# Kernel optimization log

Hardware: AMD Instinct MI355X
Metric: run time of the kernel (lower is better)

The kernel has to match this reference:

```python
import jax, jax.numpy as jnp
import numpy as np

H = 8          # n_channels
NEIGHBORS = 5


def setup_inputs() -> dict:
    key = jax.random.key(0)
    k1, k2 = jax.random.split(key)
    B, N, C = 8, 1024, 256
    x = jax.random.normal(k1, (B, N, C), dtype=jnp.float32)
    # torch Linear weight: [out_features, in_features] = [2*H*C, C]
    W_qk = jax.random.normal(k2, (2 * H * C, C), dtype=jnp.float32) * (C ** -0.5)
    return {"x": x, "W_qk": W_qk}


def _forward(x, W_qk):
    B, N, C = x.shape
    scale = C ** -0.5
    qk = (x @ W_qk.T).reshape(B, N, 2, H, C).transpose(2, 0, 3, 1, 4)
    q, k = qk[0], qk[1]                              # [B,H,N,C]
    attn = jax.nn.softmax(jnp.einsum('bhnc,bhmc->bhnm', q, k) * scale, axis=-1)

    # clip(): top-k on detached channel-summed attention
    sum_edge = jnp.sum(jax.lax.stop_gradient(attn), axis=1)   # [B,N,N]
    _, index = jax.lax.top_k(sum_edge, NEIGHBORS)             # [B,N,NEIGHBORS]
    # Faithful to source: every mask row gets 1 at the union of ALL rows'
    # top-k indices (inner loop iterates over all rows of `inds`), plus eye(N).
    flat_idx = index.reshape(B, N * NEIGHBORS)                # [B, N*nb]
    col_mask = jnp.zeros((B, N), dtype=attn.dtype).at[
        jnp.arange(B)[:, None], flat_idx].set(1.0)            # [B,N]
    mask = jnp.maximum(jnp.eye(N, dtype=attn.dtype)[None], col_mask[:, None, :])  # [B,N,N]

    new_edge = mask[:, None] * attn                           # [B,H,N,N]

    # norm_edge(): row norm, then col norm, then row @ col^T
    norm_row = new_edge / (jnp.sum(new_edge, axis=-1, keepdims=True) + 1e-16)
    norm_col = norm_row / (jnp.sum(norm_row, axis=-2, keepdims=True) + 1e-16)
    return jnp.einsum('bhnm,bhkm->bhnk', norm_row, norm_col)  # [B,H,N,N]


def reference(x, W_qk):
    return _forward(x, W_qk)
```

## Files before the change

kernel.cpp:

```cpp
#include <hip/hip_runtime.h>
#include <hip/hip_bf16.h>
#include <cstdint>
#include <cstddef>

#define BB 8
#define HH 8
#define NN 1024
#define CC 256
#define YC 2048
#define NSPLIT (BB*NN*CC/4/256)

typedef __attribute__((ext_vector_type(8))) __bf16 bf16x8;
typedef __attribute__((ext_vector_type(4))) __bf16 bf16x4;
typedef __attribute__((ext_vector_type(4))) float f32x4;

__device__ inline void async16(const void* g, void* l)
{
  __builtin_amdgcn_global_load_lds(
      reinterpret_cast<const __attribute__((address_space(1))) unsigned int*>(
          reinterpret_cast<uintptr_t>(g)),
      reinterpret_cast<__attribute__((address_space(3))) unsigned int*>(
          reinterpret_cast<uintptr_t>(l)),
      16, 0, 0);
}

__device__ inline float waveMax(float v) {
#pragma unroll
  for (int o = 32; o > 0; o >>= 1) v = fmaxf(v, __shfl_xor(v, o, 64));
  return v;
}
__device__ inline float waveSum(float v) {
#pragma unroll
  for (int o = 32; o > 0; o >>= 1) v += __shfl_xor(v, o, 64);
  return v;
}

__global__ __launch_bounds__(256) void prep_kernel(
    const float* __restrict__ x, const float* __restrict__ W,
    __bf16* __restrict__ xh, __bf16* __restrict__ xl,
    __bf16* __restrict__ Th, __bf16* __restrict__ Tl)
{
  __shared__ float t[64][65];
  if (blockIdx.x < NSPLIT) {
    const int i = blockIdx.x * 256 + threadIdx.x;
    const float4 v = ((const float4*)x)[i];
    bf16x4 h, l;
    h.x = (__bf16)v.x; l.x = (__bf16)(v.x - (float)h.x);
    h.y = (__bf16)v.y; l.y = (__bf16)(v.y - (float)h.y);
    h.z = (__bf16)v.z; l.z = (__bf16)(v.z - (float)h.z);
    h.w = (__bf16)v.w; l.w = (__bf16)(v.w - (float)h.w);
    ((bf16x4*)xh)[i] = h;
    ((bf16x4*)xl)[i] = l;
    return;
  }
  const int bid = blockIdx.x - NSPLIT;
  const int z = bid >> 4;
  const int tile = bid & 15;
  const int i0 = (tile & 3) * 64, c0 = (tile >> 2) * 64;
  const float* Wb = W + ((size_t)z << 16);
  const int tr = threadIdx.x >> 6;
  const int tc = threadIdx.x & 63;
#pragma unroll
  for (int rr = 0; rr < 64; rr += 4)
    t[rr + tr][tc] = Wb[(size_t)(i0 + rr + tr) * 256 + c0 + tc];
  __syncthreads();
  __bf16* Thb = Th + ((size_t)z << 16);
  __bf16* Tlb = Tl + ((size_t)z << 16);
#pragma unroll
  for (int cc = 0; cc < 64; cc += 4) {
    const int c = cc + tr, i = tc;
    const float v = t[i][c];
    const __bf16 h = (__bf16)v;
    Thb[(size_t)(c0 + c) * 256 + i0 + i] = h;
    Tlb[(size_t)(c0 + c) * 256 + i0 + i] = (__bf16)(v - (float)h);
  }
}

__global__ __launch_bounds__(256) void pp_mfma_kernel(
    const __bf16* __restrict__ Th, const __bf16* __restrict__ Tl,
    __bf16* __restrict__ Phi, __bf16* __restrict__ Plo)
{
  const int h = blockIdx.z;
  const __bf16* Ah = Th + ((size_t)(8 + h) << 16);
  const __bf16* Al = Tl + ((size_t)(8 + h) << 16);
  const __bf16* Bh = Th + ((size_t)h << 16);
  const __bf16* Bl = Tl + ((size_t)h << 16);

  __shared__ __bf16 AsH[128 * 32], AsL[128 * 32], BsH[128 * 32], BsL[128 * 32];

  const int tid = threadIdx.x, lane = tid & 63, wid = tid >> 6;
  const int wr = wid >> 1, wc = wid & 1;
  const int bM = blockIdx.y * 128, bN = blockIdx.x * 128;

  const int srow = wid * 16 + (lane >> 2);
  const int scol = (lane & 3) * 8;
  const __bf16* gAh = Ah + (size_t)(bM + srow) * CC + scol;
  const __bf16* gAl = Al + (size_t)(bM + srow) * CC + scol;
  const __bf16* gBh = Bh + (size_t)(bN + srow) * CC + scol;
  const __bf16* gBl = Bl + (size_t)(bN + srow) * CC + scol;
  char* lAh = (char*)AsH + wid * 16 * 64;
  char* lAl = (char*)AsL + wid * 16 * 64;
  char* lBh = (char*)BsH + wid * 16 * 64;
  char* lBl = (char*)BsL + wid * 16 * 64;

  f32x4 acc[4][4];
  const f32x4 z4 = {0.f, 0.f, 0.f, 0.f};
#pragma unroll
  for (int m = 0; m < 4; ++m)
#pragma unroll
    for (int n = 0; n < 4; ++n) acc[m][n] = z4;

  for (int k0 = 0; k0 < CC; k0 += 32) {
    async16(gAh + k0, lAh); async16(gAh + k0 + 64 * CC, lAh + 64 * 64);
    async16(gAl + k0, lAl); async16(gAl + k0 + 64 * CC, lAl + 64 * 64);
    async16(gBh + k0, lBh); async16(gBh + k0 + 64 * CC, lBh + 64 * 64);
    async16(gBl + k0, lBl); async16(gBl + k0 + 64 * CC, lBl + 64 * 64);
    __syncthreads();

    bf16x8 ah[4], al[4], bh_[4], bl_[4];
    const int fb = (lane & 15) * 64 + (lane >> 4) * 16;
#pragma unroll
    for (int m = 0; m < 4; ++m) {
      ah[m] = *(const bf16x8*)((const char*)AsH + (wr * 64 + m * 16) * 64 + fb);
      al[m] = *(const bf16x8*)((const char*)AsL + (wr * 64 + m * 16) * 64 + fb);
    }
#pragma unroll
    for (int n = 0; n < 4; ++n) {
      bh_[n] = *(const bf16x8*)((const char*)BsH + (wc * 64 + n * 16) * 64 + fb);
      bl_[n] = *(const bf16x8*)((const char*)BsL + (wc * 64 + n * 16) * 64 + fb);
    }
#pragma unroll
    for (int m = 0; m < 4; ++m)
#pragma unroll
      for (int n = 0; n < 4; ++n) {
        acc[m][n] = __builtin_amdgcn_mfma_f32_16x16x32_bf16(al[m], bh_[n], acc[m][n], 0, 0, 0);
        acc[m][n] = __builtin_amdgcn_mfma_f32_16x16x32_bf16(ah[m], bl_[n], acc[m][n], 0, 0, 0);
        acc[m][n] = __builtin_amdgcn_mfma_f32_16x16x32_bf16(ah[m], bh_[n], acc[m][n], 0, 0, 0);
      }
    __syncthreads();
  }

  const int fr = lane & 15;
  const int fq = lane >> 4;
#pragma unroll
  for (int m = 0; m < 4; ++m) {
    const int row0 = h * 256 + bM + wr * 64 + m * 16 + fq * 4;
#pragma unroll
    for (int n = 0; n < 4; ++n) {
      const int col = bN + wc * 64 + n * 16 + fr;
#pragma unroll
      for (int r = 0; r < 4; ++r) {
        const float v = acc[m][n][r];
        const __bf16 hh = (__bf16)v;
        Phi[(size_t)(row0 + r) * CC + col] = hh;
        Plo[(size_t)(row0 + r) * CC + col] = (__bf16)(v - (float)hh);
      }
    }
  }
}

__global__ __launch_bounds__(256) void y_mfma_kernel(
    const __bf16* __restrict__ Ah, const __bf16* __restrict__ Al,
    const __bf16* __restrict__ Bh, const __bf16* __restrict__ Bl,
    __bf16* __restrict__ Chi, __bf16* __restrict__ Clo)
{
  __shared__ __bf16 AsH[2][128 * 32], AsL[2][128 * 32];
  __shared__ __bf16 BsH[2][128 * 32], BsL[2][128 * 32];

  const int tid = threadIdx.x, lane = tid & 63, wid = tid >> 6;
  const int wr = wid >> 1, wc = wid & 1;
  const int bM = blockIdx.y * 128, bN = blockIdx.x * 128;

  const int srow = wid * 16 + (lane >> 2);
  const int scol = (lane & 3) * 8;
  const __bf16* gAh = Ah + (size_t)(bM + srow) * CC + scol;
  const __bf16* gAl = Al + (size_t)(bM + srow) * CC + scol;
  const __bf16* gBh = Bh + (size_t)(bN + srow) * CC + scol;
  const __bf16* gBl = Bl + (size_t)(bN + srow) * CC + scol;
  const int lofs = wid * 16 * 64;

  f32x4 acc[4][4];
  const f32x4 z = {0.f, 0.f, 0.f, 0.f};
#pragma unroll
  for (int m = 0; m < 4; ++m)
#pragma unroll
    for (int n = 0; n < 4; ++n) acc[m][n] = z;

  const int fb = (lane & 15) * 64 + (lane >> 4) * 16;

#define Y_STAGE(buf, k0_)                                                      \
  do {                                                                         \
    async16(gAh + (k0_), (char*)AsH[buf] + lofs);                              \
    async16(gAh + (k0_) + 64 * CC, (char*)AsH[buf] + lofs + 64 * 64);          \
    async16(gAl + (k0_), (char*)AsL[buf] + lofs);                              \
    async16(gAl + (k0_) + 64 * CC, (char*)AsL[buf] + lofs + 64 * 64);          \
    async16(gBh + (k0_), (char*)BsH[buf] + lofs);                              \
    async16(gBh + (k0_) + 64 * CC, (char*)BsH[buf] + lofs + 64 * 64);          \
    async16(gBl + (k0_), (char*)BsL[buf] + lofs);                              \
    async16(gBl + (k0_) + 64 * CC, (char*)BsL[buf] + lofs + 64 * 64);          \
  } while (0)

#define Y_COMPUTE(buf)                                                         \
  do {                                                                         \
    bf16x8 ah[4], al[4], bh_[4], bl_[4];                                       \
    _Pragma("unroll")                                                          \
    for (int m = 0; m < 4; ++m) {                                              \
      ah[m] = *(const bf16x8*)((const char*)AsH[buf] + (wr * 64 + m * 16) * 64 + fb); \
      al[m] = *(const bf16x8*)((const char*)AsL[buf] + (wr * 64 + m * 16) * 64 + fb); \
    }                                                                          \
    _Pragma("unroll")                                                          \
    for (int n = 0; n < 4; ++n) {                                              \
      bh_[n] = *(const bf16x8*)((const char*)BsH[buf] + (wc * 64 + n * 16) * 64 + fb); \
      bl_[n] = *(const bf16x8*)((const char*)BsL[buf] + (wc * 64 + n * 16) * 64 + fb); \
    }                                                                          \
    _Pragma("unroll")                                                          \
    for (int m = 0; m < 4; ++m)                                                \
      _Pragma("unroll")                                                        \
      for (int n = 0; n < 4; ++n) {                                            \
        acc[m][n] = __builtin_amdgcn_mfma_f32_16x16x32_bf16(al[m], bh_[n], acc[m][n], 0, 0, 0); \
        acc[m][n] = __builtin_amdgcn_mfma_f32_16x16x32_bf16(ah[m], bl_[n], acc[m][n], 0, 0, 0); \
        acc[m][n] = __builtin_amdgcn_mfma_f32_16x16x32_bf16(ah[m], bh_[n], acc[m][n], 0, 0, 0); \
      }                                                                        \
  } while (0)

  Y_STAGE(0, 0);
  int cur = 0;
#pragma unroll 1
  for (int k0 = 0; k0 < CC - 32; k0 += 32) {
    Y_STAGE(cur ^ 1, k0 + 32);
    asm volatile("s_waitcnt vmcnt(8)" ::: "memory");
    __builtin_amdgcn_s_barrier();
    __builtin_amdgcn_sched_barrier(0);
    Y_COMPUTE(cur);
    __builtin_amdgcn_s_barrier();
    __builtin_amdgcn_sched_barrier(0);
    cur ^= 1;
  }
  asm volatile("s_waitcnt vmcnt(0)" ::: "memory");
  __builtin_amdgcn_s_barrier();
  __builtin_amdgcn_sched_barrier(0);
  Y_COMPUTE(cur);

#undef Y_STAGE
#undef Y_COMPUTE

  const int fr = lane & 15;
  const int fq = lane >> 4;
#pragma unroll
  for (int m = 0; m < 4; ++m) {
    const int row0 = bM + wr * 64 + m * 16 + fq * 4;
#pragma unroll
    for (int n = 0; n < 4; ++n) {
      const int col = bN + wc * 64 + n * 16 + fr;
#pragma unroll
      for (int r = 0; r < 4; ++r) {
        const float v = acc[m][n][r];
        const __bf16 h = (__bf16)v;
        Chi[(size_t)(row0 + r) * YC + col] = h;
        Clo[(size_t)(row0 + r) * YC + col] = (__bf16)(v - (float)h);
      }
    }
  }
}

__global__ __launch_bounds__(256) void qkt_mfma_kernel(
    const __bf16* __restrict__ Yh, const __bf16* __restrict__ Yl,
    const __bf16* __restrict__ Xh, const __bf16* __restrict__ Xl,
    float* __restrict__ outall)
{
  const int f = blockIdx.x;
  const int xcd = f & 7;
  const int g = f >> 3;
  const int bh = xcd + 8 * (g >> 6);
  const int tile = g & 63;
  const int b = bh >> 3, h = bh & 7;
  const size_t aoff = (size_t)b * NN * YC + (size_t)h * CC;
  const size_t boff = (size_t)b * NN * CC;
  float* C = outall + ((size_t)bh << 20);

  __shared__ __bf16 AsH[2][128 * 32], AsL[2][128 * 32];
  __shared__ __bf16 BsH[2][128 * 32], BsL[2][128 * 32];

  const int tid = threadIdx.x, lane = tid & 63, wid = tid >> 6;
  const int wr = wid >> 1, wc = wid & 1;
  const int bM = (tile >> 3) * 128, bN = (tile & 7) * 128;

  const int srow = wid * 16 + (lane >> 2);
  const int scol = (lane & 3) * 8;
  const __bf16* gAh = Yh + aoff + (size_t)(bM + srow) * YC + scol;
  const __bf16* gAl = Yl + aoff + (size_t)(bM + srow) * YC + scol;
  const __bf16* gBh = Xh + boff + (size_t)(bN + srow) * CC + scol;
  const __bf16* gBl = Xl + boff + (size_t)(bN + srow) * CC + scol;
  const int lofs = wid * 16 * 64;

  f32x4 acc[4][4];
  const f32x4 z = {0.f, 0.f, 0.f, 0.f};
#pragma unroll
  for (int m = 0; m < 4; ++m)
#pragma unroll
    for (int n = 0; n < 4; ++n) acc[m][n] = z;

  const int fb = (lane & 15) * 64 + (lane >> 4) * 16;

#define QKT_STAGE(buf, k0_)                                                    \
  do {                                                                         \
    async16(gAh + (k0_), (char*)AsH[buf] + lofs);                              \
    async16(gAh + (k0_) + (size_t)64 * YC, (char*)AsH[buf] + lofs + 64 * 64);  \
    async16(gAl + (k0_), (char*)AsL[buf] + lofs);                              \
    async16(gAl + (k0_) + (size_t)64 * YC, (char*)AsL[buf] + lofs + 64 * 64);  \
    async16(gBh + (k0_), (char*)BsH[buf] + lofs);                              \
    async16(gBh + (k0_) + (size_t)64 * CC, (char*)BsH[buf] + lofs + 64 * 64);  \
    async16(gBl + (k0_), (char*)BsL[buf] + lofs);                              \
    async16(gBl + (k0_) + (size_t)64 * CC, (char*)BsL[buf] + lofs + 64 * 64);  \
  } while (0)

#define QKT_COMPUTE(buf)                                                       \
  do {                                                                         \
    bf16x8 ah[4], al[4], bh_[4], bl_[4];                                       \
    _Pragma("unroll")                                                          \
    for (int m = 0; m < 4; ++m) {                                              \
      ah[m] = *(const bf16x8*)((const char*)AsH[buf] + (wr * 64 + m * 16) * 64 + fb); \
      al[m] = *(const bf16x8*)((const char*)AsL[buf] + (wr * 64 + m * 16) * 64 + fb); \
    }                                                                          \
    _Pragma("unroll")                                                          \
    for (int n = 0; n < 4; ++n) {                                              \
      bh_[n] = *(const bf16x8*)((const char*)BsH[buf] + (wc * 64 + n * 16) * 64 + fb); \
      bl_[n] = *(const bf16x8*)((const char*)BsL[buf] + (wc * 64 + n * 16) * 64 + fb); \
    }                                                                          \
    _Pragma("unroll")                                                          \
    for (int m = 0; m < 4; ++m)                                                \
      _Pragma("unroll")                                                        \
      for (int n = 0; n < 4; ++n) {                                            \
        acc[m][n] = __builtin_amdgcn_mfma_f32_16x16x32_bf16(al[m], bh_[n], acc[m][n], 0, 0, 0); \
        acc[m][n] = __builtin_amdgcn_mfma_f32_16x16x32_bf16(ah[m], bl_[n], acc[m][n], 0, 0, 0); \
        acc[m][n] = __builtin_amdgcn_mfma_f32_16x16x32_bf16(ah[m], bh_[n], acc[m][n], 0, 0, 0); \
      }                                                                        \
  } while (0)

  QKT_STAGE(0, 0);
  int cur = 0;
#pragma unroll 1
  for (int k0 = 0; k0 < CC - 32; k0 += 32) {
    QKT_STAGE(cur ^ 1, k0 + 32);
    asm volatile("s_waitcnt vmcnt(8)" ::: "memory");
    __builtin_amdgcn_s_barrier();
    __builtin_amdgcn_sched_barrier(0);
    QKT_COMPUTE(cur);
    __builtin_amdgcn_s_barrier();
    __builtin_amdgcn_sched_barrier(0);
    cur ^= 1;
  }
  asm volatile("s_waitcnt vmcnt(0)" ::: "memory");
  __builtin_amdgcn_s_barrier();
  __builtin_amdgcn_sched_barrier(0);
  QKT_COMPUTE(cur);

#undef QKT_STAGE
#undef QKT_COMPUTE

  const int fr = lane & 15;
  const int fq = lane >> 4;
#pragma unroll
  for (int m = 0; m < 4; ++m) {
    const int row0 = bM + wr * 64 + m * 16 + fq * 4;
#pragma unroll
    for (int n = 0; n < 4; ++n) {
      const int col = bN + wc * 64 + n * 16 + fr;
#pragma unroll
      for (int r = 0; r < 4; ++r)
        C[(size_t)(row0 + r) * NN + col] = acc[m][n][r] * 0.0625f;
    }
  }
}

__global__ __launch_bounds__(256) void softmax_se_kernel(const float* __restrict__ logits,
                                                         __bf16* __restrict__ attnb,
                                                         float* __restrict__ se)
{
  const int bn = blockIdx.x;
  const int b = bn >> 10;
  const int n = bn & 1023;
  const int t = threadIdx.x;
  const int lane = t & 63, wv = t >> 6;
  __shared__ float wred[4];
  float4 acc = make_float4(0.f, 0.f, 0.f, 0.f);

#pragma unroll 1
  for (int h = 0; h < HH; ++h) {
    const size_t rowbase = (((size_t)(b * HH + h) << 10) + n) << 10;
    const float* ar = logits + rowbase;
    __bf16* arb = attnb + rowbase;
    float4 x = *(const float4*)(ar + (t << 2));
    float mx = waveMax(fmaxf(fmaxf(x.x, x.y), fmaxf(x.z, x.w)));
    if (lane == 0) wred[wv] = mx;
    __syncthreads();
    const float M = fmaxf(fmaxf(wred[0], wred[1]), fmaxf(wred[2], wred[3]));
    __syncthreads();

    float e0 = expf(x.x - M), e1 = expf(x.y - M), e2 = expf(x.z - M), e3 = expf(x.w - M);
    float s = waveSum(e0 + e1 + e2 + e3);
    if (lane == 0) wred[wv] = s;
    __syncthreads();
    const float inv = 1.0f / (wred[0] + wred[1] + wred[2] + wred[3]);

    const float o0 = e0 * inv, o1 = e1 * inv, o2 = e2 * inv, o3 = e3 * inv;
    bf16x4 ob; ob.x = (__bf16)o0; ob.y = (__bf16)o1; ob.z = (__bf16)o2; ob.w = (__bf16)o3;
    *(bf16x4*)(arb + (t << 2)) = ob;
    acc.x += o0; acc.y += o1; acc.z += o2; acc.w += o3;
    __syncthreads();
  }
  *(float4*)(se + (size_t)bn * NN + (t << 2)) = acc;
}

__global__ __launch_bounds__(256) void topk_kernel(const float* __restrict__ se,
                                                   float* __restrict__ colmask)
{
  const int bn = blockIdx.x;
  const int b = bn >> 10;
  const int t = threadIdx.x;
  const int lane = t & 63, wv = t >> 6;
  __shared__ float vals[NN];
  __shared__ unsigned long long wbest[4];
  const float* rowp = se + (size_t)bn * NN;
  for (int i = t; i < NN; i += 256) vals[i] = rowp[i];
  __syncthreads();

  for (int it = 0; it < 5; ++it) {
    unsigned long long best = 0ull;
    for (int i = t; i < NN; i += 256) {
      const float v = vals[i];
      if (v >= 0.f) {
        unsigned long long key =
            ((unsigned long long)__float_as_uint(v) << 32) | (unsigned)(NN - 1 - i);
        if (key > best) best = key;
      }
    }
#pragma unroll
    for (int o = 32; o > 0; o >>= 1) {
      const unsigned long long other = __shfl_xor(best, o, 64);
      if (other > best) best = other;
    }
    if (lane == 0) wbest[wv] = best;
    __syncthreads();
    if (t == 0) {
      unsigned long long bb = wbest[0];
      if (wbest[1] > bb) bb = wbest[1];
      if (wbest[2] > bb) bb = wbest[2];
      if (wbest[3] > bb) bb = wbest[3];
      const int idx = NN - 1 - (int)(bb & 0xFFFFFFFFull);
      colmask[b * NN + idx] = 1.0f;
      vals[idx] = -1.0f;
    }
    __syncthreads();
  }
}

__global__ __launch_bounds__(256) void cs_rs_kernel(const __bf16* __restrict__ attnb,
                                                    const float* __restrict__ colmask,
                                                    float* __restrict__ inv_rs,
                                                    float* __restrict__ part)
{
  const int bh = blockIdx.y;
  const int b = bh >> 3;
  const int chunk = blockIdx.x;
  const int t = threadIdx.x, lane = t & 63, wv = t >> 6;
  const __bf16* ab = attnb + ((size_t)bh << 20);
  const float* cm = colmask + b * NN;
  const int c0 = lane * 16;

  float cmv[16];
#pragma unroll
  for (int q = 0; q < 4; ++q) {
    const float4 c4 = *(const float4*)(cm + c0 + q * 4);
    cmv[q*4+0] = c4.x; cmv[q*4+1] = c4.y; cmv[q*4+2] = c4.z; cmv[q*4+3] = c4.w;
  }

  float a[16];
#pragma unroll
  for (int j = 0; j < 16; ++j) a[j] = 0.f;

  const int nbase = chunk * 64 + wv * 16;
#pragma unroll 1
  for (int r = 0; r < 16; ++r) {
    const int n = nbase + r;
    const __bf16* rowp = ab + ((size_t)n << 10) + c0;
    const bf16x8 v0 = *(const bf16x8*)(rowp);
    const bf16x8 v1 = *(const bf16x8*)(rowp + 8);
    float e[16];
    float rsum = 0.f;
#pragma unroll
    for (int j = 0; j < 8; ++j) {
      const float val = ((cmv[j] != 0.f) || (c0 + j == n)) ? (float)v0[j] : 0.f;
      e[j] = val; rsum += val;
    }
#pragma unroll
    for (int j = 0; j < 8; ++j) {
      const float val = ((cmv[8+j] != 0.f) || (c0 + 8 + j == n)) ? (float)v1[j] : 0.f;
      e[8+j] = val; rsum += val;
    }
    rsum = waveSum(rsum);
    const float ir = 1.0f / (rsum + 1e-16f);
    if (lane == 0) inv_rs[bh * NN + n] = ir;
#pragma unroll
    for (int j = 0; j < 16; ++j) a[j] += e[j] * ir;
  }

  __shared__ float l[4][NN];
#pragma unroll
  for (int j = 0; j < 16; ++j) l[wv][c0 + j] = a[j];
  __syncthreads();
  const int m0 = t << 2;
  float4 o;
  o.x = l[0][m0+0] + l[1][m0+0] + l[2][m0+0] + l[3][m0+0];
  o.y = l[0][m0+1] + l[1][m0+1] + l[2][m0+1] + l[3][m0+1];
  o.z = l[0][m0+2] + l[1][m0+2] + l[2][m0+2] + l[3][m0+2];
  o.w = l[0][m0+3] + l[1][m0+3] + l[2][m0+3] + l[3][m0+3];
  *(float4*)(part + (((size_t)chunk * (BB*HH) + bh) << 10) + m0) = o;
}

__global__ __launch_bounds__(256) void cs_fin_kernel(const float* __restrict__ part,
                                                     float* __restrict__ isc)
{
  const int bh = blockIdx.x;
  const int m0 = threadIdx.x << 2;
  float a0 = 0.f, a1 = 0.f, a2 = 0.f, a3 = 0.f;
#pragma unroll
  for (int c = 0; c < 16; ++c) {
    const float4 p = *(const float4*)(part + (((size_t)c * (BB*HH) + bh) << 10) + m0);
    a0 += p.x; a1 += p.y; a2 += p.z; a3 += p.w;
  }
  float4 o;
  o.x = 1.0f / sqrtf(a0 + 1e-16f);
  o.y = 1.0f / sqrtf(a1 + 1e-16f);
  o.z = 1.0f / sqrtf(a2 + 1e-16f);
  o.w = 1.0f / sqrtf(a3 + 1e-16f);
  *(float4*)(isc + ((size_t)bh << 10) + m0) = o;
}

__global__ __launch_bounds__(256) void g_kernel(const __bf16* __restrict__ attnb,
                                                const float* __restrict__ colmask,
                                                const float* __restrict__ inv_rs,
                                                const float* __restrict__ isc,
                                                __bf16* __restrict__ Gb)
{
  const size_t idx = ((size_t)blockIdx.x * 256 + threadIdx.x) << 3;
  const size_t row = idx >> 10;
  const int m = (int)(idx & 1023);
  const int n = (int)(row & 1023);
  const int bh = (int)(row >> 10);
  const int b = bh >> 3;
  const bf16x8 vb = *(const bf16x8*)(attnb + idx);
  const float4 c0 = *(const float4*)(colmask + b * NN + m);
  const float4 c1 = *(const float4*)(colmask + b * NN + m + 4);
  const float4 s0 = *(const float4*)(isc + ((size_t)bh << 10) + m);
  const float4 s1 = *(const float4*)(isc + ((size_t)bh << 10) + m + 4);
  const float ir = inv_rs[row];
  const float cm[8] = {c0.x, c0.y, c0.z, c0.w, c1.x, c1.y, c1.z, c1.w};
  const float sc[8] = {s0.x, s0.y, s0.z, s0.w, s1.x, s1.y, s1.z, s1.w};
  bf16x8 o;
#pragma unroll
  for (int j = 0; j < 8; ++j) {
    const float e = ((cm[j] != 0.f) || (m + j == n)) ? (float)vb[j] : 0.f;
    o[j] = (__bf16)(e * ir * sc[j]);
  }
  *(bf16x8*)(Gb + idx) = o;
}

__global__ __launch_bounds__(256) void ggt_mfma_kernel(const __bf16* __restrict__ Gball,
                                                       float* __restrict__ outall)
{
  const int f = blockIdx.x;
  const int xcd = f & 7;
  const int g = f >> 3;
  const int bh = xcd + 8 * (g / 36);
  int tt = g % 36;

  const __bf16* A = Gball + ((size_t)bh << 20);
  float* C = outall + ((size_t)bh << 20);

  int ti = 0;
#pragma unroll
  for (int r = 0; r < 8; ++r) {
    const int len = 8 - r;
    if (tt < len) { ti = r; break; }
    tt -= len;
  }
  const int tj = ti + tt;

  __shared__ __bf16 As[2][128 * 32];
  __shared__ __bf16 Bs[2][128 * 32];

  const int tid  = threadIdx.x;
  const int lane = tid & 63;
  const int wid  = tid >> 6;
  const int wr   = wid >> 1;
  const int wc   = wid & 1;
  const int bM   = ti * 128;
  const int bN   = tj * 128;

  const int srow = wid * 16 + (lane >> 2);
  const int scol = (lane & 3) * 8;
  const __bf16* gA = A + (size_t)(bM + srow) * NN + scol;
  const __bf16* gB = A + (size_t)(bN + srow) * NN + scol;
  const int lofs = wid * 16 * 64;

  f32x4 acc[4][4];
  const f32x4 z = {0.f, 0.f, 0.f, 0.f};
#pragma unroll
  for (int m = 0; m < 4; ++m)
#pragma unroll
    for (int n = 0; n < 4; ++n) acc[m][n] = z;

  const int fb = (lane & 15) * 64 + (lane >> 4) * 16;

  async16(gA,           (char*)As[0] + lofs);
  async16(gA + 64 * NN, (char*)As[0] + lofs + 64 * 64);
  async16(gB,           (char*)Bs[0] + lofs);
  async16(gB + 64 * NN, (char*)Bs[0] + lofs + 64 * 64);

  int cur = 0;
#pragma unroll 1
  for (int k0 = 0; k0 < NN - 32; k0 += 32) {
    const int nxt = cur ^ 1;
    async16(gA + k0 + 32,           (char*)As[nxt] + lofs);
    async16(gA + k0 + 32 + 64 * NN, (char*)As[nxt] + lofs + 64 * 64);
    async16(gB + k0 + 32,           (char*)Bs[nxt] + lofs);
    async16(gB + k0 + 32 + 64 * NN, (char*)Bs[nxt] + lofs + 64 * 64);
    asm volatile("s_waitcnt vmcnt(4)" ::: "memory");
    __builtin_amdgcn_s_barrier();
    __builtin_amdgcn_sched_barrier(0);

    bf16x8 a[4], b[4];
#pragma unroll
    for (int m = 0; m < 4; ++m)
      a[m] = *(const bf16x8*)((const char*)As[cur] + (wr * 64 + m * 16) * 64 + fb);
#pragma unroll
    for (int n = 0; n < 4; ++n)
      b[n] = *(const bf16x8*)((const char*)Bs[cur] + (wc * 64 + n * 16) * 64 + fb);
#pragma unroll
    for (int m = 0; m < 4; ++m)
#pragma unroll
      for (int n = 0; n < 4; ++n)
        acc[m][n] = __builtin_amdgcn_mfma_f32_16x16x32_bf16(a[m], b[n], acc[m][n], 0, 0, 0);
    __builtin_amdgcn_s_barrier();
    __builtin_amdgcn_sched_barrier(0);
    cur ^= 1;
  }

  asm volatile("s_waitcnt vmcnt(0)" ::: "memory");
  __builtin_amdgcn_s_barrier();
  __builtin_amdgcn_sched_barrier(0);
  {
    bf16x8 a[4], b[4];
#pragma unroll
    for (int m = 0; m < 4; ++m)
      a[m] = *(const bf16x8*)((const char*)As[cur] + (wr * 64 + m * 16) * 64 + fb);
#pragma unroll
    for (int n = 0; n < 4; ++n)
      b[n] = *(const bf16x8*)((const char*)Bs[cur] + (wc * 64 + n * 16) * 64 + fb);
#pragma unroll
    for (int m = 0; m < 4; ++m)
#pragma unroll
      for (int n = 0; n < 4; ++n)
        acc[m][n] = __builtin_amdgcn_mfma_f32_16x16x32_bf16(a[m], b[n], acc[m][n], 0, 0, 0);
  }

  const int fr = lane & 15;
  const int fq = lane >> 4;
#pragma unroll
  for (int m = 0; m < 4; ++m) {
    const int row0 = bM + wr * 64 + m * 16 + fq * 4;
#pragma unroll
    for (int n = 0; n < 4; ++n) {
      const int col = bN + wc * 64 + n * 16 + fr;
#pragma unroll
      for (int r = 0; r < 4; ++r)
        C[(size_t)(row0 + r) * NN + col] = acc[m][n][r];
    }
  }
  if (ti != tj) {
#pragma unroll
    for (int m = 0; m < 4; ++m) {
      const int colT = bM + wr * 64 + m * 16 + fq * 4;
#pragma unroll
      for (int n = 0; n < 4; ++n) {
        const int rowT = bN + wc * 64 + n * 16 + fr;
        *(f32x4*)(C + (size_t)rowT * NN + colT) = acc[m][n];
      }
    }
  }
}

extern "C" void kernel_launch(void* const* d_in, const int* in_sizes, int n_in,
                              void* d_out, int out_size, void* d_ws, size_t ws_size,
                              hipStream_t stream)
{
  const float* x = (const float*)d_in[0];
  const float* W = (const float*)d_in[1];
  float* logits = (float*)d_out;
  char* ws = (char*)d_ws;

  __bf16* y_hi  = (__bf16*)(ws + ((size_t)0   << 20));
  __bf16* y_lo  = (__bf16*)(ws + ((size_t)32  << 20));
  __bf16* attnb = (__bf16*)(ws + ((size_t)0   << 20));
  __bf16* x_hi  = (__bf16*)(ws + ((size_t)128 << 20));
  __bf16* x_lo  = (__bf16*)(ws + ((size_t)132 << 20));
  __bf16* T_hi  = (__bf16*)(ws + ((size_t)136 << 20));
  __bf16* T_lo  = (__bf16*)(ws + ((size_t)138 << 20));
  __bf16* P_hi  = (__bf16*)(ws + ((size_t)140 << 20));
  __bf16* P_lo  = (__bf16*)(ws + ((size_t)142 << 20));
  float*  se    = (float*)(ws + ((size_t)144 << 20));
  float*  cmask = (float*)(ws + ((size_t)176 << 20));
  float*  irs   = (float*)(ws + ((size_t)177 << 20));
  float*  isc   = (float*)(ws + ((size_t)178 << 20));
  float*  csp   = (float*)(ws + ((size_t)180 << 20));
  __bf16* Gb    = (__bf16*)(ws + ((size_t)192 << 20));

  hipLaunchKernelGGL(prep_kernel, dim3(NSPLIT + 256), dim3(256), 0, stream,
                     x, W, x_hi, x_lo, T_hi, T_lo);
  hipLaunchKernelGGL(pp_mfma_kernel, dim3(2, 2, 8), dim3(256), 0, stream,
                     T_hi, T_lo, P_hi, P_lo);

  hipLaunchKernelGGL(y_mfma_kernel, dim3(YC/128, (BB*NN)/128, 1), dim3(256), 0, stream,
                     x_hi, x_lo, P_hi, P_lo, y_hi, y_lo);

  hipLaunchKernelGGL(qkt_mfma_kernel, dim3(64 * 64), dim3(256), 0, stream,
                     y_hi, y_lo, x_hi, x_lo, logits);

  hipLaunchKernelGGL(softmax_se_kernel, dim3(BB*NN), dim3(256), 0, stream,
                     logits, attnb, se);

  hipMemsetAsync(cmask, 0, (size_t)BB * NN * 4, stream);
  hipLaunchKernelGGL(topk_kernel, dim3(BB*NN), dim3(256), 0, stream, se, cmask);

  hipLaunchKernelGGL(cs_rs_kernel, dim3(16, BB*HH), dim3(256), 0, stream,
                     attnb, cmask, irs, csp);
  hipLaunchKernelGGL(cs_fin_kernel, dim3(BB*HH), dim3(256), 0, stream, csp, isc);

  hipLaunchKernelGGL(g_kernel, dim3((BB*HH*NN*(long long)NN) / 8 / 256), dim3(256), 0, stream,
                     attnb, cmask, irs, isc, Gb);

  hipLaunchKernelGGL(ggt_mfma_kernel, dim3(36 * 64), dim3(256), 0, stream,
                     Gb, logits);

  (void)in_sizes; (void)n_in; (void)out_size; (void)ws_size;
}
```

Baseline: 512.7 us.

## Widen QK^T tile to 128x256 and drop LDS double buffering

The QK^T logits kernel moves from 128x128 to 128x256 output tiles, halving the grid and doubling the per-wave accumulators (4x8 fragments). This raises reuse of the A tile from LDS and cuts redundant global loads. To fit, the two-stage async LDS pipeline is replaced by a single buffer with plain __syncthreads before and after compute. Global load latency is therefore no longer overlapped with MFMA work, and register pressure rises, which may lower occupancy.

```diff
diff --git a/kernel.cpp b/kernel.cpp
--- a/kernel.cpp
+++ b/kernel.cpp
@@ -271,19 +271,19 @@
   const int f = blockIdx.x;
   const int xcd = f & 7;
   const int g = f >> 3;
-  const int bh = xcd + 8 * (g >> 6);
-  const int tile = g & 63;
+  const int bh = xcd + 8 * (g >> 5);
+  const int tile = g & 31;
   const int b = bh >> 3, h = bh & 7;
   const size_t aoff = (size_t)b * NN * YC + (size_t)h * CC;
   const size_t boff = (size_t)b * NN * CC;
   float* C = outall + ((size_t)bh << 20);
 
-  __shared__ __bf16 AsH[2][128 * 32], AsL[2][128 * 32];
-  __shared__ __bf16 BsH[2][128 * 32], BsL[2][128 * 32];
+  __shared__ __bf16 AsH[128 * 32], AsL[128 * 32];
+  __shared__ __bf16 BsH[256 * 32], BsL[256 * 32];
 
   const int tid = threadIdx.x, lane = tid & 63, wid = tid >> 6;
   const int wr = wid >> 1, wc = wid & 1;
-  const int bM = (tile >> 3) * 128, bN = (tile & 7) * 128;
+  const int bM = (tile >> 2) * 128, bN = (tile & 3) * 256;
 
   const int srow = wid * 16 + (lane >> 2);
   const int scol = (lane & 3) * 8;
@@ -291,72 +291,60 @@
   const __bf16* gAl = Yl + aoff + (size_t)(bM + srow) * YC + scol;
   const __bf16* gBh = Xh + boff + (size_t)(bN + srow) * CC + scol;
   const __bf16* gBl = Xl + boff + (size_t)(bN + srow) * CC + scol;
-  const int lofs = wid * 16 * 64;
-
-  f32x4 acc[4][4];
+  char* lAh = (char*)AsH + wid * 16 * 64;
+  char* lAl = (char*)AsL + wid * 16 * 64;
+  char* lBh = (char*)BsH + wid * 16 * 64;
+  char* lBl = (char*)BsL + wid * 16 * 64;
+
+  f32x4 acc[4][8];
   const f32x4 z = {0.f, 0.f, 0.f, 0.f};
 #pragma unroll
   for (int m = 0; m < 4; ++m)
 #pragma unroll
-    for (int n = 0; n < 4; ++n) acc[m][n] = z;
+    for (int n = 0; n < 8; ++n) acc[m][n] = z;
 
   const int fb = (lane & 15) * 64 + (lane >> 4) * 16;
 
-#define QKT_STAGE(buf, k0_)                                                    \
-  do {                                                                         \
-    async16(gAh + (k0_), (char*)AsH[buf] + lofs);                              \
-    async16(gAh + (k0_) + (size_t)64 * YC, (char*)AsH[buf] + lofs + 64 * 64);  \
-    async16(gAl + (k0_), (char*)AsL[buf] + lofs);                              \
-    async16(gAl + (k0_) + (size_t)64 * YC, (char*)AsL[buf] + lofs + 64 * 64);  \
-    async16(gBh + (k0_), (char*)BsH[buf] + lofs);                              \
-    async16(gBh + (k0_) + (size_t)64 * CC, (char*)BsH[buf] + lofs + 64 * 64);  \
-    async16(gBl + (k0_), (char*)BsL[buf] + lofs);                              \
-    async16(gBl + (k0_) + (size_t)64 * CC, (char*)BsL[buf] + lofs + 64 * 64);  \
-  } while (0)
-
-#define QKT_COMPUTE(buf)                                                       \
-  do {                                                                         \
-    bf16x8 ah[4], al[4], bh_[4], bl_[4];                                       \
-    _Pragma("unroll")                                                          \
-    for (int m = 0; m < 4; ++m) {                                              \
-      ah[m] = *(const bf16x8*)((const char*)AsH[buf] + (wr * 64 + m * 16) * 64 + fb); \
-      al[m] = *(const bf16x8*)((const char*)AsL[buf] + (wr * 64 + m * 16) * 64 + fb); \
-    }                                                                          \
-    _Pragma("unroll")                                                          \
-    for (int n = 0; n < 4; ++n) {                                              \
-      bh_[n] = *(const bf16x8*)((const char*)BsH[buf] + (wc * 64 + n * 16) * 64 + fb); \
-      bl_[n] = *(const bf16x8*)((const char*)BsL[buf] + (wc * 64 + n * 16) * 64 + fb); \
-    }                                                                          \
-    _Pragma("unroll")                                                          \
-    for (int m = 0; m < 4; ++m)                                                \
-      _Pragma("unroll")                                                        \
-      for (int n = 0; n < 4; ++n) {                                            \
-        acc[m][n] = __builtin_amdgcn_mfma_f32_16x16x32_bf16(al[m], bh_[n], acc[m][n], 0, 0, 0); \
-        acc[m][n] = __builtin_amdgcn_mfma_f32_16x16x32_bf16(ah[m], bl_[n], acc[m][n], 0, 0, 0); \
-        acc[m][n] = __builtin_amdgcn_mfma_f32_16x16x32_bf16(ah[m], bh_[n], acc[m][n], 0, 0, 0); \
-      }                                                                        \
-  } while (0)
-
-  QKT_STAGE(0, 0);
-  int cur = 0;
 #pragma unroll 1
-  for (int k0 = 0; k0 < CC - 32; k0 += 32) {
-    QKT_STAGE(cur ^ 1, k0 + 32);
-    asm volatile("s_waitcnt vmcnt(8)" ::: "memory");
-    __builtin_amdgcn_s_barrier();
-    __builtin_amdgcn_sched_barrier(0);
-    QKT_COMPUTE(cur);
-    __builtin_amdgcn_s_barrier();
-    __builtin_amdgcn_sched_barrier(0);
-    cur ^= 1;
-  }
-  asm volatile("s_waitcnt vmcnt(0)" ::: "memory");
-  __builtin_amdgcn_s_barrier();
-  __builtin_amdgcn_sched_barrier(0);
-  QKT_COMPUTE(cur);
-
-#undef QKT_STAGE
-#undef QKT_COMPUTE
+  for (int k0 = 0; k0 < CC; k0 += 32) {
+    async16(gAh + k0, lAh);
+    async16(gAh + k0 + (size_t)64 * YC, lAh + 64 * 64);
+    async16(gAl + k0, lAl);
+    async16(gAl + k0 + (size_t)64 * YC, lAl + 64 * 64);
+#pragma unroll
+    for (int j = 0; j < 4; ++j) {
+      async16(gBh + k0 + (size_t)(j * 64) * CC, lBh + j * 64 * 64);
+      async16(gBl + k0 + (size_t)(j * 64) * CC, lBl + j * 64 * 64);
+    }
+    __syncthreads();
+
+    bf16x8 ah[4], al[4];
+#pragma unroll
+    for (int m = 0; m < 4; ++m) {
+      ah[m] = *(const bf16x8*)((const char*)AsH + (wr * 64 + m * 16) * 64 + fb);
+      al[m] = *(const bf16x8*)((const char*)AsL + (wr * 64 + m * 16) * 64 + fb);
+    }
+#pragma unroll
+    for (int half = 0; half < 2; ++half) {
+      bf16x8 bh_[4], bl_[4];
+#pragma unroll
+      for (int n = 0; n < 4; ++n) {
+        const int row = wc * 128 + half * 64 + n * 16;
+        bh_[n] = *(const bf16x8*)((const char*)BsH + row * 64 + fb);
+        bl_[n] = *(const bf16x8*)((const char*)BsL + row * 64 + fb);
+      }
+#pragma unroll
+      for (int m = 0; m < 4; ++m)
+#pragma unroll
+        for (int n = 0; n < 4; ++n) {
+          const int nn = half * 4 + n;
+          acc[m][nn] = __builtin_amdgcn_mfma_f32_16x16x32_bf16(al[m], bh_[n], acc[m][nn], 0, 0, 0);
+          acc[m][nn] = __builtin_amdgcn_mfma_f32_16x16x32_bf16(ah[m], bl_[n], acc[m][nn], 0, 0, 0);
+          acc[m][nn] = __builtin_amdgcn_mfma_f32_16x16x32_bf16(ah[m], bh_[n], acc[m][nn], 0, 0, 0);
+        }
+    }
+    __syncthreads();
+  }
 
   const int fr = lane & 15;
   const int fq = lane >> 4;
@@ -364,8 +352,8 @@
   for (int m = 0; m < 4; ++m) {
     const int row0 = bM + wr * 64 + m * 16 + fq * 4;
 #pragma unroll
-    for (int n = 0; n < 4; ++n) {
-      const int col = bN + wc * 64 + n * 16 + fr;
+    for (int n = 0; n < 8; ++n) {
+      const int col = bN + wc * 128 + n * 16 + fr;
 #pragma unroll
       for (int r = 0; r < 4; ++r)
         C[(size_t)(row0 + r) * NN + col] = acc[m][n][r] * 0.0625f;
@@ -724,7 +712,7 @@
   hipLaunchKernelGGL(y_mfma_kernel, dim3(YC/128, (BB*NN)/128, 1), dim3(256), 0, stream,
                      x_hi, x_lo, P_hi, P_lo, y_hi, y_lo);
 
-  hipLaunchKernelGGL(qkt_mfma_kernel, dim3(64 * 64), dim3(256), 0, stream,
+  hipLaunchKernelGGL(qkt_mfma_kernel, dim3(64 * 32), dim3(256), 0, stream,
                      y_hi, y_lo, x_hi, x_lo, logits);
 
   hipLaunchKernelGGL(softmax_se_kernel, dim3(BB*NN), dim3(256), 0, stream,
```

Measured after the change: 560.3 us. 1.09x slower.
